# Kernel tuning notes

Measured on AMD Instinct MI355X. Metric: run time of the kernel, lower is better.

The kernel has to match this reference:

```python
import jax, jax.numpy as jnp
import numpy as np

N_NODES = 50000
NEG_SLOPE = 0.2  # PyG GATv2Conv default negative_slope


def _gatv2_layer(x, src, dst, W_l, W_r, att, bias, num_nodes):
    """Single-head GATv2Conv (PyG semantics, flow source_to_target)."""
    x_l = x @ W_l  # [N, C] source-side transform
    x_r = x @ W_r  # [N, C] target-side transform
    h = x_l[src] + x_r[dst]                      # [E, C] per-edge pre-activation
    h = jnp.where(h > 0, h, NEG_SLOPE * h)       # LeakyReLU
    e = h @ att                                  # [E] unnormalized attention logits
    # segment softmax over destination nodes (stable)
    e_max = jax.ops.segment_max(e, dst, num_segments=num_nodes)
    e_exp = jnp.exp(e - e_max[dst])
    denom = jax.ops.segment_sum(e_exp, dst, num_segments=num_nodes)
    alpha = e_exp / denom[dst]                   # [E]
    out = jax.ops.segment_sum(x_l[src] * alpha[:, None], dst, num_segments=num_nodes)
    return out + bias, alpha


def setup_inputs() -> dict:
    key = jax.random.key(0)
    ks = jax.random.split(key, 12)
    N, E, T, D = N_NODES, 800000, 512, 128
    g = lambda k, shp, fan_in: jax.random.normal(k, shp, dtype=jnp.float32) / np.sqrt(fan_in)
    return {
        "x": jax.random.normal(ks[0], (N, T), dtype=jnp.float32),
        "edge_index": jax.random.randint(ks[1], (2, E), 0, N, dtype=jnp.int64 if jax.config.jax_enable_x64 else jnp.int32),
        "mmse_score": jax.random.uniform(ks[2], (1,), dtype=jnp.float32),
        "W_l1": g(ks[3], (T, D), T),
        "W_r1": g(ks[4], (T, D), T),
        "att1": g(ks[5], (D,), D),
        "bias1": jnp.zeros((D,), jnp.float32),
        "W_l2": g(ks[6], (D, D), D),
        "W_r2": g(ks[7], (D, D), D),
        "att2": g(ks[8], (D,), D),
        "bias2": jnp.zeros((D,), jnp.float32),
        "mmse_W": g(ks[9], (1, D), 1),
        "mmse_b": jnp.zeros((D,), jnp.float32),
    }


def reference(x, edge_index, mmse_score, W_l1, W_r1, att1, bias1,
              W_l2, W_r2, att2, bias2, mmse_W, mmse_b):
    N = x.shape[0]
    # PyG add_self_loops=True: append one self-loop per node
    loops = jnp.arange(N, dtype=edge_index.dtype)
    src = jnp.concatenate([edge_index[0], loops])
    dst = jnp.concatenate([edge_index[1], loops])

    attn_features1, attn_weights = _gatv2_layer(x, src, dst, W_l1, W_r1, att1, bias1, N)
    # attn_weights is detached in the original (torch.tensor(...)); layer 2 ignores
    # the passed edge_attr (edge_dim=None -> no lin_edge) and recomputes attention.
    attn_weights = jax.lax.stop_gradient(attn_weights)
    graph_features, _ = _gatv2_layer(attn_features1, src, dst, W_l2, W_r2, att2, bias2, N)
    mmse_embedded = mmse_score @ mmse_W + mmse_b  # [D]
    graph_features = graph_features + mmse_embedded
    return graph_features, attn_weights
```

## Files before the change

kernel.cpp:

```cpp
#include <hip/hip_runtime.h>
#include <cstdint>

typedef __bf16 bf16;
typedef __bf16 bf16x8 __attribute__((ext_vector_type(8)));
typedef float f32x4 __attribute__((ext_vector_type(4)));

__device__ __forceinline__ void load_lds16(const void* g, void* l) {
  __builtin_amdgcn_global_load_lds(
      (const __attribute__((address_space(1))) void*)g,
      (__attribute__((address_space(3))) void*)l, 16, 0, 0);
}

__device__ __forceinline__ unsigned short bf16_bits(float f) {
  return __builtin_bit_cast(unsigned short, (bf16)f);
}
__device__ __forceinline__ float bf_lo(unsigned u) {
  return __uint_as_float(u << 16);
}
__device__ __forceinline__ float bf_hi(unsigned u) {
  return __uint_as_float(u & 0xffff0000u);
}

__global__ void hist_kernel(const int* __restrict__ ei, int E, int N,
                            int* __restrict__ counts) {
  const int total = E + N;
  for (int i = blockIdx.x * blockDim.x + threadIdx.x; i < total;
       i += gridDim.x * blockDim.x) {
    const int d = (i < E) ? ei[E + i] : (i - E);
    atomicAdd(&counts[d], 1);
  }
}

__global__ void scan_reduce(const int* __restrict__ counts,
                            int* __restrict__ bsum, int N) {
  __shared__ int red[256];
  const int chunk = (N + 255) / 256;
  const int lo = blockIdx.x * chunk;
  const int hi = min(lo + chunk, N);
  int s = 0;
  for (int i = lo + threadIdx.x; i < hi; i += 256) s += counts[i];
  red[threadIdx.x] = s;
  __syncthreads();
  for (int off = 128; off; off >>= 1) {
    if (threadIdx.x < off) red[threadIdx.x] += red[threadIdx.x + off];
    __syncthreads();
  }
  if (threadIdx.x == 0) bsum[blockIdx.x] = red[0];
}

__global__ void scan_bsum(int* __restrict__ bsum, int* __restrict__ row_ptr,
                          int N) {
  __shared__ int tmp[256];
  const int tid = threadIdx.x;
  const int v = bsum[tid];
  tmp[tid] = v;
  __syncthreads();
  for (int off = 1; off < 256; off <<= 1) {
    const int t = (tid >= off) ? tmp[tid - off] : 0;
    __syncthreads();
    tmp[tid] += t;
    __syncthreads();
  }
  bsum[tid] = tmp[tid] - v;
  if (tid == 255) row_ptr[N] = tmp[255];
}

__global__ void scan_write(const int* __restrict__ counts,
                           const int* __restrict__ boff,
                           int* __restrict__ row_ptr, int* __restrict__ cursor,
                           int N) {
  __shared__ int tmp[256];
  const int chunk = (N + 255) / 256;
  const int lo = blockIdx.x * chunk;
  const int hi = min(lo + chunk, N);
  int carry = boff[blockIdx.x];
  for (int base = lo; base < hi; base += 256) {
    const int i = base + threadIdx.x;
    const int v = (i < hi) ? counts[i] : 0;
    tmp[threadIdx.x] = v;
    __syncthreads();
    for (int off = 1; off < 256; off <<= 1) {
      const int t = (threadIdx.x >= off) ? tmp[threadIdx.x - off] : 0;
      __syncthreads();
      tmp[threadIdx.x] += t;
      __syncthreads();
    }
    if (i < hi) {
      const int excl = carry + tmp[threadIdx.x] - v;
      row_ptr[i] = excl;
      cursor[i] = excl;
    }
    carry += tmp[255];
    __syncthreads();
  }
}

__global__ void scatter_kernel(const int* __restrict__ ei, int E, int N,
                               int* __restrict__ cursor,
                               int* __restrict__ csr_src,
                               int* __restrict__ pos_of) {
  const int total = E + N;
  for (int i = blockIdx.x * blockDim.x + threadIdx.x; i < total;
       i += gridDim.x * blockDim.x) {
    int s, d;
    if (i < E) { s = ei[i]; d = ei[E + i]; } else { s = d = i - E; }
    const int pos = atomicAdd(&cursor[d], 1);
    csr_src[pos] = s;
    pos_of[i] = pos;
  }
}

__global__ void mmse_kernel(const float* __restrict__ score,
                            const float* __restrict__ W,
                            const float* __restrict__ b,
                            float* __restrict__ out, int D) {
  const int i = threadIdx.x;
  if (i < D) out[i] = score[0] * W[i] + b[i];
}

__global__ void wt_kernel(const float* __restrict__ Wl,
                          const float* __restrict__ Wr,
                          bf16* __restrict__ Wt, int K) {
  const int idx = blockIdx.x * blockDim.x + threadIdx.x;
  if (idx >= 256 * K) return;
  const int col = idx & 255;
  const int k = idx >> 8;
  const float v = (col < 128) ? Wl[k * 128 + col] : Wr[k * 128 + (col - 128)];
  Wt[(size_t)col * K + k] = (bf16)v;
}

template <bool AF32>
__global__ __launch_bounds__(512) void gemm_mfma(
    const void* __restrict__ Ap, const bf16* __restrict__ Wt,
    bf16* __restrict__ xl, bf16* __restrict__ xr, int M, int K) {
  __shared__ __align__(16) bf16 Alds[128 * 32];
  __shared__ __align__(16) bf16 Blds[256 * 32];

  const int tid = threadIdx.x;
  const int w = tid >> 6, lane = tid & 63;
  const int wr = w >> 2, wc = w & 3;
  const int row0 = blockIdx.x * 128;

  const int s_row = tid >> 2;
  const int s_k = (tid & 3) * 8;
  const int a_row = min(row0 + s_row, M - 1);
  bf16* a_dst = Alds + tid * 8;

  const int b_col0 = w * 32 + (lane >> 2);
  const bf16* b_src0 = Wt + (size_t)b_col0 * K + (lane & 3) * 8;
  const bf16* b_src1 = Wt + (size_t)(b_col0 + 16) * K + (lane & 3) * 8;
  bf16* b_dst0 = Blds + w * 1024 + lane * 8;
  bf16* b_dst1 = b_dst0 + 512;

  const int a_f0 = (wr * 64 + (lane & 15)) * 32 + (lane >> 4) * 8;
  const int b_f0 = (wc * 64 + (lane & 15)) * 32 + (lane >> 4) * 8;

  f32x4 acc[4][4] = {};

  for (int k0 = 0; k0 < K; k0 += 32) {
    bf16x8 av;
    if (AF32) {
      const float* A = (const float*)Ap;
      const float4 f0 = *(const float4*)&A[(size_t)a_row * K + k0 + s_k];
      const float4 f1 = *(const float4*)&A[(size_t)a_row * K + k0 + s_k + 4];
      av[0] = (bf16)f0.x; av[1] = (bf16)f0.y; av[2] = (bf16)f0.z; av[3] = (bf16)f0.w;
      av[4] = (bf16)f1.x; av[5] = (bf16)f1.y; av[6] = (bf16)f1.z; av[7] = (bf16)f1.w;
    } else {
      av = *(const bf16x8*)((const bf16*)Ap + (size_t)a_row * K + k0 + s_k);
    }
    __syncthreads();
    *(bf16x8*)a_dst = av;
    load_lds16(b_src0 + k0, b_dst0);
    load_lds16(b_src1 + k0, b_dst1);
    __syncthreads();

    bf16x8 af[4], bfr[4];
#pragma unroll
    for (int m = 0; m < 4; ++m) af[m] = *(const bf16x8*)(Alds + a_f0 + m * 512);
#pragma unroll
    for (int n = 0; n < 4; ++n) bfr[n] = *(const bf16x8*)(Blds + b_f0 + n * 512);
#pragma unroll
    for (int m = 0; m < 4; ++m)
#pragma unroll
      for (int n = 0; n < 4; ++n)
        acc[m][n] = __builtin_amdgcn_mfma_f32_16x16x32_bf16(af[m], bfr[n],
                                                            acc[m][n], 0, 0, 0);
  }

#pragma unroll
  for (int m = 0; m < 4; ++m) {
    const int rbase = row0 + wr * 64 + m * 16 + (lane >> 4) * 4;
#pragma unroll
    for (int n = 0; n < 4; ++n) {
      const int c = wc * 64 + n * 16 + (lane & 15);
      bf16* dst = (c < 128) ? xl : xr;
      const int cc = c & 127;
#pragma unroll
      for (int j = 0; j < 4; ++j) {
        const int r = rbase + j;
        if (r < M) dst[(size_t)r * 128 + cc] = (bf16)acc[m][n][j];
      }
    }
  }
}

__global__ __launch_bounds__(256) void gat_edge(
    const bf16* __restrict__ xl, const bf16* __restrict__ xr,
    const int* __restrict__ row_ptr, const int* __restrict__ csr_src,
    const float* __restrict__ att, const float* __restrict__ bias,
    const float* __restrict__ extra,
    bf16* __restrict__ out_b,
    float* __restrict__ out_f,
    float* __restrict__ e_ws, float* __restrict__ m_ws,
    float* __restrict__ den_ws, int N) {
  const int wave = threadIdx.x >> 6;
  const int lane = threadIdx.x & 63;
  const int l5 = lane & 31;
  const int half = lane >> 5;
  const int node_raw = blockIdx.x * 8 + wave * 2 + half;
  const bool vnode = node_raw < N;
  const int node = vnode ? node_raw : N - 1;

  const int d0 = l5 * 4;
  const float4 attv = *(const float4*)&att[d0];
  const uint2 ur = *(const uint2*)&xr[(size_t)node * 128 + d0];
  const float r0 = bf_lo(ur.x), r1 = bf_hi(ur.x);
  const float r2 = bf_lo(ur.y), r3 = bf_hi(ur.y);

  float m = -1e30f, den = 0.f;
  float a0 = 0.f, a1 = 0.f, a2 = 0.f, a3 = 0.f;

  const int beg = vnode ? row_ptr[node] : 0;
  const int end = vnode ? row_ptr[node + 1] : 0;
  const int nbat = (end - beg + 7) >> 3;
  const int nloop = max(nbat, __shfl_xor(nbat, 32));
  const int nloop2 = (nloop + 1) & ~1;

  int sA[8], sB[8];
  uint2 uA[8], uB[8];

  auto load_idx = [&](int b, int* s) {
#pragma unroll
    for (int j = 0; j < 8; ++j) {
      const int k = beg + b * 8 + j;
      s[j] = csr_src[(k < end) ? k : beg];
    }
  };
  auto gather = [&](const int* s, uint2* u) {
#pragma unroll
    for (int j = 0; j < 8; ++j)
      u[j] = *(const uint2*)&xl[(size_t)s[j] * 128 + d0];
  };
  auto compute = [&](int b, const uint2* u) {
    const int idx = beg + b * 8;
    float p[8];
#pragma unroll
    for (int j = 0; j < 8; ++j) {
      float h0 = bf_lo(u[j].x) + r0;
      float h1 = bf_hi(u[j].x) + r1;
      float h2 = bf_lo(u[j].y) + r2;
      float h3 = bf_hi(u[j].y) + r3;
      h0 = h0 > 0.f ? h0 : 0.2f * h0;
      h1 = h1 > 0.f ? h1 : 0.2f * h1;
      h2 = h2 > 0.f ? h2 : 0.2f * h2;
      h3 = h3 > 0.f ? h3 : 0.2f * h3;
      p[j] = fmaf(h0, attv.x, fmaf(h1, attv.y, fmaf(h2, attv.z, h3 * attv.w)));
    }
#pragma unroll
    for (int off = 16; off; off >>= 1) {
#pragma unroll
      for (int j = 0; j < 8; ++j) p[j] += __shfl_xor(p[j], off);
    }
#pragma unroll
    for (int j = 0; j < 8; ++j)
      if (idx + j >= end) p[j] = -1e30f;

    if (e_ws != nullptr && l5 == 0) {
#pragma unroll
      for (int j = 0; j < 8; ++j)
        if (idx + j < end) e_ws[idx + j] = p[j];
    }

    const float bm = fmaxf(fmaxf(fmaxf(p[0], p[1]), fmaxf(p[2], p[3])),
                           fmaxf(fmaxf(p[4], p[5]), fmaxf(p[6], p[7])));
    if (bm > m) {
      const float f = __expf(m - bm);
      den *= f;
      a0 *= f; a1 *= f; a2 *= f; a3 *= f;
      m = bm;
    }
#pragma unroll
    for (int j = 0; j < 8; ++j) {
      const float wgt = __expf(p[j] - m);
      den += wgt;
      a0 = fmaf(wgt, bf_lo(u[j].x), a0);
      a1 = fmaf(wgt, bf_hi(u[j].x), a1);
      a2 = fmaf(wgt, bf_lo(u[j].y), a2);
      a3 = fmaf(wgt, bf_hi(u[j].y), a3);
    }
  };

  load_idx(0, sA);
  gather(sA, uA);
  load_idx(1, sB);

  for (int t = 0; t < nloop2; t += 2) {
    gather(sB, uB);
    load_idx(t + 2, sA);
    compute(t, uA);
    gather(sA, uA);
    load_idx(t + 3, sB);
    compute(t + 1, uB);
  }

  if (!vnode) return;

  const float inv = 1.f / den;
  const float4 bv = *(const float4*)&bias[d0];
  float o0 = fmaf(a0, inv, bv.x);
  float o1 = fmaf(a1, inv, bv.y);
  float o2 = fmaf(a2, inv, bv.z);
  float o3 = fmaf(a3, inv, bv.w);
  if (extra != nullptr) {
    const float4 ev = *(const float4*)&extra[d0];
    o0 += ev.x; o1 += ev.y; o2 += ev.z; o3 += ev.w;
  }
  if (out_b != nullptr) {
    uint2 pk;
    pk.x = (unsigned)bf16_bits(o0) | ((unsigned)bf16_bits(o1) << 16);
    pk.y = (unsigned)bf16_bits(o2) | ((unsigned)bf16_bits(o3) << 16);
    *(uint2*)&out_b[(size_t)node * 128 + d0] = pk;
  }
  if (out_f != nullptr) {
    float4 ov; ov.x = o0; ov.y = o1; ov.z = o2; ov.w = o3;
    *(float4*)&out_f[(size_t)node * 128 + d0] = ov;
  }
  if (m_ws != nullptr && l5 == 0) {
    m_ws[node] = m;
    den_ws[node] = den;
  }
}

__global__ void alpha_kernel(const float* __restrict__ e_ws,
                             const float* __restrict__ m_ws,
                             const float* __restrict__ den_ws,
                             const int* __restrict__ ei,
                             const int* __restrict__ pos_of, int E, int N,
                             float* __restrict__ out_alpha) {
  const int i = blockIdx.x * blockDim.x + threadIdx.x;
  if (i >= E + N) return;
  const int d = (i < E) ? ei[E + i] : (i - E);
  const int pos = pos_of[i];
  out_alpha[i] = __expf(e_ws[pos] - m_ws[d]) / den_ws[d];
}

extern "C" void kernel_launch(void* const* d_in, const int* in_sizes, int n_in,
                              void* d_out, int out_size, void* d_ws,
                              size_t ws_size, hipStream_t stream) {
  const float* x          = (const float*)d_in[0];
  const int*   ei         = (const int*)d_in[1];
  const float* mmse_score = (const float*)d_in[2];
  const float* W_l1       = (const float*)d_in[3];
  const float* W_r1       = (const float*)d_in[4];
  const float* att1       = (const float*)d_in[5];
  const float* bias1      = (const float*)d_in[6];
  const float* W_l2       = (const float*)d_in[7];
  const float* W_r2       = (const float*)d_in[8];
  const float* att2       = (const float*)d_in[9];
  const float* bias2      = (const float*)d_in[10];
  const float* mmse_W     = (const float*)d_in[11];
  const float* mmse_b     = (const float*)d_in[12];

  const int D  = in_sizes[5];
  const int T  = in_sizes[3] / D;
  const int N  = in_sizes[0] / T;
  const int E  = in_sizes[1] / 2;
  const int ET = E + N;

  char* wptr = (char*)d_ws;
  auto alloc = [&](size_t bytes) {
    char* p = wptr;
    wptr += (bytes + 255) & ~(size_t)255;
    return p;
  };
  bf16* xl      = (bf16*)alloc((size_t)N * 128 * 2);
  bf16* xr      = (bf16*)alloc((size_t)N * 128 * 2);
  bf16* attn1   = (bf16*)alloc((size_t)N * 128 * 2);
  bf16* Wt1     = (bf16*)alloc((size_t)256 * T * 2);
  bf16* Wt2     = (bf16*)alloc((size_t)256 * D * 2);
  float* e_ws   = (float*)alloc((size_t)ET * 4);
  float* m_ws   = (float*)alloc((size_t)N * 4);
  float* den_ws = (float*)alloc((size_t)N * 4);
  float* mmse_vec = (float*)alloc(512);
  int* counts  = (int*)alloc((size_t)N * 4);
  int* row_ptr = (int*)alloc((size_t)(N + 1) * 4);
  int* cursor  = (int*)alloc((size_t)N * 4);
  int* bsum    = (int*)alloc(256 * 4);
  int* csr_src = (int*)alloc((size_t)ET * 4);
  int* pos_of  = (int*)alloc((size_t)ET * 4);

  float* out_feat  = (float*)d_out;
  float* out_alpha = out_feat + (size_t)N * D;

  hipMemsetAsync(counts, 0, (size_t)N * 4, stream);
  hist_kernel<<<2048, 256, 0, stream>>>(ei, E, N, counts);
  scan_reduce<<<256, 256, 0, stream>>>(counts, bsum, N);
  scan_bsum<<<1, 256, 0, stream>>>(bsum, row_ptr, N);
  scan_write<<<256, 256, 0, stream>>>(counts, bsum, row_ptr, cursor, N);
  scatter_kernel<<<2048, 256, 0, stream>>>(ei, E, N, cursor, csr_src, pos_of);

  wt_kernel<<<(256 * T + 255) / 256, 256, 0, stream>>>(W_l1, W_r1, Wt1, T);
  wt_kernel<<<(256 * D + 255) / 256, 256, 0, stream>>>(W_l2, W_r2, Wt2, D);
  mmse_kernel<<<1, 128, 0, stream>>>(mmse_score, mmse_W, mmse_b, mmse_vec, D);

  const int gblocks = (N + 127) / 128;
  gemm_mfma<true><<<gblocks, 512, 0, stream>>>(x, Wt1, xl, xr, N, T);

  gat_edge<<<(N + 7) / 8, 256, 0, stream>>>(xl, xr, row_ptr, csr_src, att1,
                                            bias1, nullptr, attn1, nullptr,
                                            e_ws, m_ws, den_ws, N);

  alpha_kernel<<<(ET + 255) / 256, 256, 0, stream>>>(e_ws, m_ws, den_ws, ei,
                                                     pos_of, E, N, out_alpha);

  gemm_mfma<false><<<gblocks, 512, 0, stream>>>(attn1, Wt2, xl, xr, N, D);

  gat_edge<<<(N + 7) / 8, 256, 0, stream>>>(xl, xr, row_ptr, csr_src, att2,
                                            bias2, mmse_vec, nullptr, out_feat,
                                            nullptr, nullptr, nullptr, N);
}
```

Baseline: 509.2 us.

## Drop software prefetch pipeline in gat_edge and raise occupancy via launch bounds

New measurement: 759.7 us. 1.49x slower.

```diff
diff --git a/kernel.cpp b/kernel.cpp
--- a/kernel.cpp
+++ b/kernel.cpp
@@ -204,7 +204,7 @@
   }
 }
 
-__global__ __launch_bounds__(256) void gat_edge(
+__global__ __launch_bounds__(256, 8) void gat_edge(
     const bf16* __restrict__ xl, const bf16* __restrict__ xr,
     const int* __restrict__ row_ptr, const int* __restrict__ csr_src,
     const float* __restrict__ att, const float* __restrict__ bias,
@@ -234,25 +234,18 @@
   const int end = vnode ? row_ptr[node + 1] : 0;
   const int nbat = (end - beg + 7) >> 3;
   const int nloop = max(nbat, __shfl_xor(nbat, 32));
-  const int nloop2 = (nloop + 1) & ~1;
-
-  int sA[8], sB[8];
-  uint2 uA[8], uB[8];
-
-  auto load_idx = [&](int b, int* s) {
+
+  for (int t = 0; t < nloop; ++t) {
+    const int idx = beg + t * 8;
+
+    uint2 u[8];
 #pragma unroll
     for (int j = 0; j < 8; ++j) {
-      const int k = beg + b * 8 + j;
-      s[j] = csr_src[(k < end) ? k : beg];
-    }
-  };
-  auto gather = [&](const int* s, uint2* u) {
-#pragma unroll
-    for (int j = 0; j < 8; ++j)
-      u[j] = *(const uint2*)&xl[(size_t)s[j] * 128 + d0];
-  };
-  auto compute = [&](int b, const uint2* u) {
-    const int idx = beg + b * 8;
+      const int k = idx + j;
+      const int s = csr_src[(k < end) ? k : beg];
+      u[j] = *(const uint2*)&xl[(size_t)s * 128 + d0];
+    }
+
     float p[8];
 #pragma unroll
     for (int j = 0; j < 8; ++j) {
@@ -260,17 +253,19 @@
       float h1 = bf_hi(u[j].x) + r1;
       float h2 = bf_lo(u[j].y) + r2;
       float h3 = bf_hi(u[j].y) + r3;
-      h0 = h0 > 0.f ? h0 : 0.2f * h0;
-      h1 = h1 > 0.f ? h1 : 0.2f * h1;
-      h2 = h2 > 0.f ? h2 : 0.2f * h2;
-      h3 = h3 > 0.f ? h3 : 0.2f * h3;
+      h0 = fmaxf(h0, 0.2f * h0);
+      h1 = fmaxf(h1, 0.2f * h1);
+      h2 = fmaxf(h2, 0.2f * h2);
+      h3 = fmaxf(h3, 0.2f * h3);
       p[j] = fmaf(h0, attv.x, fmaf(h1, attv.y, fmaf(h2, attv.z, h3 * attv.w)));
     }
+
 #pragma unroll
     for (int off = 16; off; off >>= 1) {
 #pragma unroll
       for (int j = 0; j < 8; ++j) p[j] += __shfl_xor(p[j], off);
     }
+
 #pragma unroll
     for (int j = 0; j < 8; ++j)
       if (idx + j >= end) p[j] = -1e30f;
@@ -298,19 +293,6 @@
       a2 = fmaf(wgt, bf_lo(u[j].y), a2);
       a3 = fmaf(wgt, bf_hi(u[j].y), a3);
     }
-  };
-
-  load_idx(0, sA);
-  gather(sA, uA);
-  load_idx(1, sB);
-
-  for (int t = 0; t < nloop2; t += 2) {
-    gather(sB, uB);
-    load_idx(t + 2, sA);
-    compute(t, uA);
-    gather(sA, uA);
-    load_idx(t + 3, sB);
-    compute(t + 1, uB);
   }
 
   if (!vnode) return;
```
